# Optimization experiments

Hardware: AMD Instinct MI355X
Metric: run time of the kernel (lower is better)

Reference implementation:

```python
import jax, jax.numpy as jnp
import numpy as np

N_NODES = 50000
N_EDGES = 800000
N_PAIRS = 200000
IN_DIM = 128
HID = 64
OUT_DIM = 1


def _gat_layer(x, W, a_l, a_r, src, dst, n_nodes):
    # Single-head GAT (DGL-style): z = xW; attention logits from learned
    # left/right vectors; softmax over incoming edges of each dst node.
    z = x @ W                                   # [N, H]
    el = z @ a_l                                # [N]
    er = z @ a_r                                # [N]
    e = jax.nn.leaky_relu(el[src] + er[dst], 0.2)   # [E]
    emax = jax.ops.segment_max(e, dst, num_segments=n_nodes)  # [N]
    ex = jnp.exp(e - emax[dst])                 # [E], stable softmax numerator
    denom = jax.ops.segment_sum(ex, dst, num_segments=n_nodes)  # [N]
    msg = ex[:, None] * z[src]                  # [E, H]
    agg = jax.ops.segment_sum(msg, dst, num_segments=n_nodes)   # [N, H]
    return agg / jnp.maximum(denom, 1e-9)[:, None]


def setup_inputs() -> dict:
    key = jax.random.key(0)
    ks = jax.random.split(key, 10)
    feat = jax.random.normal(ks[0], (N_NODES, IN_DIM), dtype=jnp.float32)
    src = jax.random.randint(ks[1], (N_EDGES,), 0, N_NODES, dtype=jnp.int32)
    dst = jax.random.randint(ks[2], (N_EDGES,), 0, N_NODES, dtype=jnp.int32)
    # query pairs: take existing edges so the has_edges_between mask is true
    pair_src = src[:N_PAIRS]
    pair_dst = dst[:N_PAIRS]
    s1 = 1.0 / np.sqrt(IN_DIM)
    s2 = 1.0 / np.sqrt(HID)
    W1 = jax.random.normal(ks[3], (IN_DIM, HID), dtype=jnp.float32) * s1
    al1 = jax.random.normal(ks[4], (HID,), dtype=jnp.float32) * s2
    ar1 = jax.random.normal(ks[5], (HID,), dtype=jnp.float32) * s2
    W2 = jax.random.normal(ks[6], (HID, HID), dtype=jnp.float32) * s2
    al2 = jax.random.normal(ks[7], (HID,), dtype=jnp.float32) * s2
    ar2 = jax.random.normal(ks[8], (HID,), dtype=jnp.float32) * s2
    Wc = jax.random.normal(ks[9], (2 * HID, OUT_DIM), dtype=jnp.float32) * s2
    bc = jnp.zeros((OUT_DIM,), dtype=jnp.float32)
    return {"feat": feat, "W1": W1, "al1": al1, "ar1": ar1,
            "W2": W2, "al2": al2, "ar2": ar2, "Wc": Wc, "bc": bc,
            "src": src, "dst": dst, "pair_src": pair_src, "pair_dst": pair_dst}


def reference(feat, W1, al1, ar1, W2, al2, ar2, Wc, bc, src, dst, pair_src, pair_dst):
    src = src.astype(jnp.int32)
    dst = dst.astype(jnp.int32)
    # two hetero GAT layers (single ntype -> mean aggregate is identity) + ReLU
    h = jax.nn.relu(_gat_layer(feat, W1, al1, ar1, src, dst, N_NODES))
    h = jax.nn.relu(_gat_layer(h, W2, al2, ar2, src, dst, N_NODES))
    # has_edges_between(pair_src, pair_dst): membership test via sorted edge keys
    ekeys = src.astype(jnp.int64) * N_NODES + dst.astype(jnp.int64)
    skeys = jnp.sort(ekeys)
    pkeys = pair_src.astype(jnp.int64) * N_NODES + pair_dst.astype(jnp.int64)
    idx = jnp.clip(jnp.searchsorted(skeys, pkeys), 0, N_EDGES - 1)
    mask = (skeys[idx] == pkeys)                 # [P] bool
    # gather endpoint embeddings, concat, classify, sigmoid; invalid rows -> 0
    hs = h[pair_src]                             # [P, H]
    hd = h[pair_dst]                             # [P, H]
    h_pair = jnp.concatenate([hs, hd], axis=1)   # [P, 2H]
    out = jax.nn.sigmoid(h_pair @ Wc + bc)       # [P, OUT]
    return out * mask[:, None].astype(out.dtype)
```

## Files before the change

### kernel.cpp

```cpp
#include <hip/hip_runtime.h>
#include <cstdint>

#define N_NODES 50000
#define N_EDGES 800000
#define N_PAIRS 200000
#define IN_DIM 128
#define HID 64
#define N_WAVES_GEMM (N_NODES / 16)
#define NB1 196
#define CHUNK ((N_EDGES + NB1 - 1) / NB1)
#define MHIST (NB1 * NB1)
#define SBG ((MHIST + 255) / 256)

typedef __attribute__((ext_vector_type(8))) short bf16x8;
typedef __attribute__((ext_vector_type(4))) float f32x4;

__device__ __forceinline__ unsigned short bf16_rne(float f) {
    unsigned u = __float_as_uint(f);
    unsigned t = u + 0x7FFFu + ((u >> 16) & 1u);
    return (unsigned short)(t >> 16);
}
__device__ __forceinline__ void bf2f(unsigned u, float& a, float& b) {
    a = __uint_as_float(u << 16);
    b = __uint_as_float(u & 0xFFFF0000u);
}

__global__ __launch_bounds__(256) void hist_prep(
    const int* __restrict__ dst, int* __restrict__ histHi,
    const float* __restrict__ W1, const float* __restrict__ W2,
    unsigned short* __restrict__ w1hi, unsigned short* __restrict__ w1lo,
    unsigned short* __restrict__ w2hi, unsigned short* __restrict__ w2lo)
{
    const int t = threadIdx.x, b = blockIdx.x;
    if (b < NB1) {
        __shared__ int hist[256];
        hist[t] = 0; __syncthreads();
        const int beg = b * CHUNK, end = min(beg + CHUNK, N_EDGES);
        for (int e = beg + t; e < end; e += 256) atomicAdd(&hist[dst[e] >> 8], 1);
        __syncthreads();
        if (t < NB1) histHi[t * NB1 + b] = hist[t];
    } else {
        int tid = (b - NB1) * 256 + t;
        if (tid < 8192) {
            int jj = tid & 7, lane = (tid >> 3) & 63, tt = (tid >> 9) & 3, ks = tid >> 11;
            int k = ks * 32 + (lane >> 4) * 8 + jj;
            int n = tt * 16 + (lane & 15);
            float f = W1[k * HID + n];
            unsigned short hi = bf16_rne(f);
            float fhi = __uint_as_float(((unsigned)hi) << 16);
            w1hi[tid] = hi;
            w1lo[tid] = bf16_rne(f - fhi);
        }
        if (tid < 4096) {
            int jj = tid & 7, lane = (tid >> 3) & 63, tt = (tid >> 9) & 3, ks = tid >> 11;
            int k = ks * 32 + (lane >> 4) * 8 + jj;
            int n = tt * 16 + (lane & 15);
            float f = W2[k * HID + n];
            unsigned short hi = bf16_rne(f);
            float fhi = __uint_as_float(((unsigned)hi) << 16);
            w2hi[tid] = hi;
            w2lo[tid] = bf16_rne(f - fhi);
        }
    }
}

__global__ __launch_bounds__(256) void gemm_mfma_f(
    const float* __restrict__ x,
    const unsigned short* __restrict__ whi, const unsigned short* __restrict__ wlo,
    const float* __restrict__ al, const float* __restrict__ ar,
    unsigned short* __restrict__ z, float* __restrict__ el, float* __restrict__ er)
{
    const int lane = threadIdx.x;
    const int wave = blockIdx.x * 4 + threadIdx.y;
    if (wave >= N_WAVES_GEMM) return;
    const int i0 = wave * 16;
    const int m = lane & 15, quad = lane >> 4;

    f32x4 acc[4] = {{0.f,0.f,0.f,0.f},{0.f,0.f,0.f,0.f},{0.f,0.f,0.f,0.f},{0.f,0.f,0.f,0.f}};
    const float* xrow = x + (size_t)(i0 + m) * IN_DIM;

    #pragma unroll 1
    for (int ks = 0; ks < 4; ++ks) {
        const float4 xv0 = *(const float4*)&xrow[ks * 32 + quad * 8];
        const float4 xv1 = *(const float4*)&xrow[ks * 32 + quad * 8 + 4];
        float xs[8] = {xv0.x, xv0.y, xv0.z, xv0.w, xv1.x, xv1.y, xv1.z, xv1.w};
        bf16x8 ahi, alo;
        #pragma unroll
        for (int jj = 0; jj < 8; ++jj) {
            unsigned short hb = bf16_rne(xs[jj]);
            float fhi = __uint_as_float(((unsigned)hb) << 16);
            ahi[jj] = (short)hb;
            alo[jj] = (short)bf16_rne(xs[jj] - fhi);
        }
        #pragma unroll
        for (int t = 0; t < 4; ++t) {
            const bf16x8 bhi = *(const bf16x8*)&whi[(((ks * 4 + t) * 64) + lane) * 8];
            const bf16x8 blo = *(const bf16x8*)&wlo[(((ks * 4 + t) * 64) + lane) * 8];
            acc[t] = __builtin_amdgcn_mfma_f32_16x16x32_bf16(ahi, bhi, acc[t], 0, 0, 0);
            acc[t] = __builtin_amdgcn_mfma_f32_16x16x32_bf16(ahi, blo, acc[t], 0, 0, 0);
            acc[t] = __builtin_amdgcn_mfma_f32_16x16x32_bf16(alo, bhi, acc[t], 0, 0, 0);
        }
    }

    #pragma unroll
    for (int r = 0; r < 4; ++r) {
        const int row = quad * 4 + r;
        float se = 0.f, sr = 0.f;
        #pragma unroll
        for (int t = 0; t < 4; ++t) {
            float v = acc[t][r];
            z[(size_t)(i0 + row) * HID + t * 16 + m] = bf16_rne(v);
            se = fmaf(v, al[t * 16 + m], se);
            sr = fmaf(v, ar[t * 16 + m], sr);
        }
        #pragma unroll
        for (int off = 1; off < 16; off <<= 1) {
            se += __shfl_xor(se, off, 64);
            sr += __shfl_xor(sr, off, 64);
        }
        if (m == 0) { el[i0 + row] = se; er[i0 + row] = sr; }
    }
}

__global__ __launch_bounds__(256) void gemm_mfma_b(
    const unsigned short* __restrict__ x,
    const unsigned short* __restrict__ whi, const unsigned short* __restrict__ wlo,
    const float* __restrict__ al, const float* __restrict__ ar,
    unsigned short* __restrict__ z, float* __restrict__ el, float* __restrict__ er)
{
    const int lane = threadIdx.x;
    const int wave = blockIdx.x * 4 + threadIdx.y;
    if (wave >= N_WAVES_GEMM) return;
    const int i0 = wave * 16;
    const int m = lane & 15, quad = lane >> 4;

    f32x4 acc[4] = {{0.f,0.f,0.f,0.f},{0.f,0.f,0.f,0.f},{0.f,0.f,0.f,0.f},{0.f,0.f,0.f,0.f}};
    const unsigned short* xrow = x + (size_t)(i0 + m) * HID;

    #pragma unroll 1
    for (int ks = 0; ks < 2; ++ks) {
        const bf16x8 a = *(const bf16x8*)&xrow[ks * 32 + quad * 8];
        #pragma unroll
        for (int t = 0; t < 4; ++t) {
            const bf16x8 bhi = *(const bf16x8*)&whi[(((ks * 4 + t) * 64) + lane) * 8];
            const bf16x8 blo = *(const bf16x8*)&wlo[(((ks * 4 + t) * 64) + lane) * 8];
            acc[t] = __builtin_amdgcn_mfma_f32_16x16x32_bf16(a, bhi, acc[t], 0, 0, 0);
            acc[t] = __builtin_amdgcn_mfma_f32_16x16x32_bf16(a, blo, acc[t], 0, 0, 0);
        }
    }

    #pragma unroll
    for (int r = 0; r < 4; ++r) {
        const int row = quad * 4 + r;
        float se = 0.f, sr = 0.f;
        #pragma unroll
        for (int t = 0; t < 4; ++t) {
            float v = acc[t][r];
            z[(size_t)(i0 + row) * HID + t * 16 + m] = bf16_rne(v);
            se = fmaf(v, al[t * 16 + m], se);
            sr = fmaf(v, ar[t * 16 + m], sr);
        }
        #pragma unroll
        for (int off = 1; off < 16; off <<= 1) {
            se += __shfl_xor(se, off, 64);
            sr += __shfl_xor(sr, off, 64);
        }
        if (m == 0) { el[i0 + row] = se; er[i0 + row] = sr; }
    }
}

__global__ __launch_bounds__(256) void scan1g(
    const int* __restrict__ in, int* __restrict__ ex, int* __restrict__ bsums, int n)
{
    __shared__ int sh[256];
    const int t = threadIdx.x;
    const int i = blockIdx.x * 256 + t;
    int v = (i < n) ? in[i] : 0;
    sh[t] = v; __syncthreads();
    #pragma unroll
    for (int off = 1; off < 256; off <<= 1) {
        int x = sh[t];
        int a = (t >= off) ? sh[t - off] : 0;
        __syncthreads();
        sh[t] = x + a;
        __syncthreads();
    }
    if (i < n) ex[i] = sh[t] - v;
    if (t == 255) bsums[blockIdx.x] = sh[255];
}

__global__ __launch_bounds__(256) void scan2g(int* __restrict__ bsums, int nb)
{
    __shared__ int sh[256];
    const int t = threadIdx.x;
    int v = (t < nb) ? bsums[t] : 0;
    sh[t] = v; __syncthreads();
    #pragma unroll
    for (int off = 1; off < 256; off <<= 1) {
        int x = sh[t];
        int a = (t >= off) ? sh[t - off] : 0;
        __syncthreads();
        sh[t] = x + a;
        __syncthreads();
    }
    if (t < nb) bsums[t] = sh[t] - v;
}

__global__ __launch_bounds__(256) void scatter_hi(
    const int* __restrict__ src, const int* __restrict__ dst,
    const int* __restrict__ histEx, const int* __restrict__ bsums,
    unsigned* __restrict__ pairs)
{
    __shared__ int base[256];
    const int t = threadIdx.x, b = blockIdx.x;
    if (t < NB1) {
        int idx = t * NB1 + b;
        base[t] = histEx[idx] + bsums[idx >> 8];
    }
    __syncthreads();
    const int beg = b * CHUNK, end = min(beg + CHUNK, N_EDGES);
    for (int e = beg + t; e < end; e += 256) {
        int s = src[e], d = dst[e];
        int pos = atomicAdd(&base[d >> 8], 1);
        pairs[pos] = ((unsigned)s << 16) | (unsigned)d;
    }
}

__global__ __launch_bounds__(256) void seg_sort(
    const unsigned* __restrict__ pairs, const int* __restrict__ histEx,
    const int* __restrict__ bsums,
    int* __restrict__ row_start, int* __restrict__ csr_src)
{
    __shared__ int hist[256], sc[256], offs[256];
    const int t = threadIdx.x, b = blockIdx.x;
    const int i0 = b * NB1;
    const int segStart = histEx[i0] + bsums[i0 >> 8];
    int segEnd = N_EDGES;
    if (b < NB1 - 1) {
        const int i1 = (b + 1) * NB1;
        segEnd = histEx[i1] + bsums[i1 >> 8];
    }
    hist[t] = 0; __syncthreads();
    for (int i = segStart + t; i < segEnd; i += 256)
        atomicAdd(&hist[pairs[i] & 255], 1);
    __syncthreads();
    int v = hist[t]; sc[t] = v; __syncthreads();
    #pragma unroll
    for (int off = 1; off < 256; off <<= 1) {
        int x = sc[t];
        int a = (t >= off) ? sc[t - off] : 0;
        __syncthreads();
        sc[t] = x + a;
        __syncthreads();
    }
    const int excl = sc[t] - v;
    offs[t] = segStart + excl;
    const int node = b * 256 + t;
    if (node <= N_NODES) row_start[node] = segStart + excl;
    __syncthreads();
    for (int i = segStart + t; i < segEnd; i += 256) {
        unsigned p = pairs[i];
        int pos = atomicAdd(&offs[p & 255], 1);
        csr_src[pos] = (int)(p >> 16);
    }
}

__global__ __launch_bounds__(256) void node_agg(
    const int* __restrict__ row_start, const int* __restrict__ csr_src,
    const float* __restrict__ el, const float* __restrict__ er,
    const unsigned short* __restrict__ z, unsigned short* __restrict__ h)
{
    const int lane = threadIdx.x;
    const int i = blockIdx.x * 4 + threadIdx.y;
    if (i >= N_NODES) return;
    const int rb = row_start[i], re = row_start[i + 1];
    const float er_i = er[i];
    const int es = lane >> 3;
    const int fl = lane & 7;

    float acc[8] = {0.f,0.f,0.f,0.f,0.f,0.f,0.f,0.f};
    float den = 0.f;

    int eA = rb + es;        bool vA = eA < re;
    int eB = eA + 8;         bool vB = eB < re;
    int sA = vA ? csr_src[eA] : 0;
    int sB = vB ? csr_src[eB] : 0;
    float elA = el[sA];
    uint4 zA = ((const uint4*)(z + (size_t)sA * HID))[fl];

    for (int e0 = rb; e0 < re; e0 += 8) {
        const int eC = e0 + 16 + es;
        const bool vC = eC < re;
        const int sC = vC ? csr_src[eC] : 0;
        const float elB = el[sB];
        const uint4 zB = ((const uint4*)(z + (size_t)sB * HID))[fl];

        float x = elA + er_i;
        float lr = x > 0.f ? x : 0.2f * x;
        float ex = vA ? __expf(lr) : 0.f;
        float z0, z1, z2, z3, z4, z5, z6, z7;
        bf2f(zA.x, z0, z1); bf2f(zA.y, z2, z3);
        bf2f(zA.z, z4, z5); bf2f(zA.w, z6, z7);
        acc[0] = fmaf(ex, z0, acc[0]); acc[1] = fmaf(ex, z1, acc[1]);
        acc[2] = fmaf(ex, z2, acc[2]); acc[3] = fmaf(ex, z3, acc[3]);
        acc[4] = fmaf(ex, z4, acc[4]); acc[5] = fmaf(ex, z5, acc[5]);
        acc[6] = fmaf(ex, z6, acc[6]); acc[7] = fmaf(ex, z7, acc[7]);
        den += ex;

        sA = sB; vA = vB; elA = elB; zA = zB;
        sB = sC; vB = vC;
    }
    #pragma unroll
    for (int off = 8; off < 64; off <<= 1) {
        #pragma unroll
        for (int q = 0; q < 8; ++q) acc[q] += __shfl_xor(acc[q], off, 64);
        den += __shfl_xor(den, off, 64);
    }
    if (es == 0) {
        float inv = 1.f / fmaxf(den, 1e-9f);
        unsigned short o[8];
        #pragma unroll
        for (int q = 0; q < 8; ++q) o[q] = bf16_rne(fmaxf(acc[q] * inv, 0.f));
        uint4 pk;
        pk.x = (unsigned)o[0] | ((unsigned)o[1] << 16);
        pk.y = (unsigned)o[2] | ((unsigned)o[3] << 16);
        pk.z = (unsigned)o[4] | ((unsigned)o[5] << 16);
        pk.w = (unsigned)o[6] | ((unsigned)o[7] << 16);
        ((uint4*)(h + (size_t)i * HID))[fl] = pk;
    }
}

__global__ __launch_bounds__(256) void pair_head(
    const int* __restrict__ ps, const int* __restrict__ pd,
    const unsigned short* __restrict__ h, const float* __restrict__ Wc,
    const float* __restrict__ bc, const int* __restrict__ row_start,
    const int* __restrict__ csr_src, float* __restrict__ out)
{
    const int lane = threadIdx.x;
    const int p = blockIdx.x * 8 + threadIdx.y * 2 + (lane >> 5);
    if (p >= N_PAIRS) return;
    const int r = lane & 31;
    const int which = r >> 4;
    const int f4 = r & 15;
    int s = ps[p], d = pd[p];
    int node = which ? d : s;
    const uint2 hv = ((const uint2*)(h + (size_t)node * HID))[f4];
    float h0, h1, h2, h3;
    bf2f(hv.x, h0, h1); bf2f(hv.y, h2, h3);
    const float4 wv = *(const float4*)&Wc[which * HID + f4 * 4];
    float v = h0 * wv.x + h1 * wv.y + h2 * wv.z + h3 * wv.w;

    const int rb = row_start[d], re = row_start[d + 1];
    int found = 0;
    for (int e = rb + r; e < re; e += 32) found |= (csr_src[e] == s) ? 1 : 0;

    #pragma unroll
    for (int off = 1; off < 32; off <<= 1) {
        v += __shfl_xor(v, off, 64);
        found |= __shfl_xor(found, off, 64);
    }
    if (r == 0) {
        float sg = 1.f / (1.f + __expf(-(v + bc[0])));
        out[p] = found ? sg : 0.f;
    }
}

extern "C" void kernel_launch(void* const* d_in, const int* in_sizes, int n_in,
                              void* d_out, int out_size, void* d_ws, size_t ws_size,
                              hipStream_t stream)
{
    const float* feat = (const float*)d_in[0];
    const float* W1   = (const float*)d_in[1];
    const float* al1  = (const float*)d_in[2];
    const float* ar1  = (const float*)d_in[3];
    const float* W2   = (const float*)d_in[4];
    const float* al2  = (const float*)d_in[5];
    const float* ar2  = (const float*)d_in[6];
    const float* Wc   = (const float*)d_in[7];
    const float* bc   = (const float*)d_in[8];
    const int* src    = (const int*)d_in[9];
    const int* dst    = (const int*)d_in[10];
    const int* psrc   = (const int*)d_in[11];
    const int* pdst   = (const int*)d_in[12];
    float* out = (float*)d_out;

    char* ws = (char*)d_ws;
    unsigned short* z  = (unsigned short*)ws;  ws += (size_t)N_NODES * HID * 2;
    unsigned short* h1 = (unsigned short*)ws;  ws += (size_t)N_NODES * HID * 2;
    float* el = (float*)ws;               ws += (size_t)N_NODES * 4;
    float* er = (float*)ws;               ws += (size_t)N_NODES * 4;
    int* row_start = (int*)ws;            ws += (size_t)(N_NODES + 1) * 4;
    int* histHi = (int*)ws;               ws += (size_t)MHIST * 4;
    int* bsumsA = (int*)ws;               ws += (size_t)(SBG + 1) * 4;
    ws = (char*)(((uintptr_t)ws + 255) & ~(uintptr_t)255);
    unsigned* pairs = (unsigned*)ws;      ws += (size_t)N_EDGES * 4;
    int* csr_src = (int*)ws;              ws += (size_t)N_EDGES * 4;
    unsigned short* w1hi = (unsigned short*)ws;  ws += 8192 * 2;
    unsigned short* w1lo = (unsigned short*)ws;  ws += 8192 * 2;
    unsigned short* w2hi = (unsigned short*)ws;  ws += 4096 * 2;
    unsigned short* w2lo = (unsigned short*)ws;  ws += 4096 * 2;

    dim3 b64x4(64, 4);
    const int MB = (N_WAVES_GEMM + 3) / 4;

    hist_prep<<<NB1 + 32, 256, 0, stream>>>(dst, histHi, W1, W2, w1hi, w1lo, w2hi, w2lo);
    scan1g<<<SBG, 256, 0, stream>>>(histHi, histHi, bsumsA, MHIST);
    scan2g<<<1, 256, 0, stream>>>(bsumsA, SBG);
    scatter_hi<<<NB1, 256, 0, stream>>>(src, dst, histHi, bsumsA, pairs);
    seg_sort<<<NB1, 256, 0, stream>>>(pairs, histHi, bsumsA, row_start, csr_src);

    gemm_mfma_f<<<MB, b64x4, 0, stream>>>(feat, w1hi, w1lo, al1, ar1, z, el, er);
    node_agg<<<(N_NODES + 3) / 4, b64x4, 0, stream>>>(row_start, csr_src, el, er, z, h1);

    gemm_mfma_b<<<MB, b64x4, 0, stream>>>(h1, w2hi, w2lo, al2, ar2, z, el, er);
    node_agg<<<(N_NODES + 3) / 4, b64x4, 0, stream>>>(row_start, csr_src, el, er, z, h1);

    pair_head<<<N_PAIRS / 8, b64x4, 0, stream>>>(psrc, pdst, h1, Wc, bc, row_start, csr_src, out);
}
```

Before: 212.9 us.

## Merge scan with first GEMM, fold classifier into aggregation, restructure pair head

```diff
diff --git a/kernel.cpp b/kernel.cpp
--- a/kernel.cpp
+++ b/kernel.cpp
@@ -11,6 +11,9 @@
 #define CHUNK ((N_EDGES + NB1 - 1) / NB1)
 #define MHIST (NB1 * NB1)
 #define SBG ((MHIST + 255) / 256)
+#define MB_GEMM ((N_WAVES_GEMM + 3) / 4)
+#define NODE_BLOCKS ((N_NODES + 3) / 4)
+#define MEMBER_BLOCKS (N_PAIRS / 32)
 
 typedef __attribute__((ext_vector_type(8))) short bf16x8;
 typedef __attribute__((ext_vector_type(4))) float f32x4;
@@ -64,18 +67,15 @@
     }
 }
 
-__global__ __launch_bounds__(256) void gemm_mfma_f(
+__device__ __forceinline__ void gemm1_body(
+    int wave, int lane,
     const float* __restrict__ x,
     const unsigned short* __restrict__ whi, const unsigned short* __restrict__ wlo,
     const float* __restrict__ al, const float* __restrict__ ar,
     unsigned short* __restrict__ z, float* __restrict__ el, float* __restrict__ er)
 {
-    const int lane = threadIdx.x;
-    const int wave = blockIdx.x * 4 + threadIdx.y;
-    if (wave >= N_WAVES_GEMM) return;
     const int i0 = wave * 16;
     const int m = lane & 15, quad = lane >> 4;
-
     f32x4 acc[4] = {{0.f,0.f,0.f,0.f},{0.f,0.f,0.f,0.f},{0.f,0.f,0.f,0.f},{0.f,0.f,0.f,0.f}};
     const float* xrow = x + (size_t)(i0 + m) * IN_DIM;
 
@@ -101,7 +101,6 @@
             acc[t] = __builtin_amdgcn_mfma_f32_16x16x32_bf16(alo, bhi, acc[t], 0, 0, 0);
         }
     }
-
     #pragma unroll
     for (int r = 0; r < 4; ++r) {
         const int row = quad * 4 + r;
@@ -122,60 +121,41 @@
     }
 }
 
-__global__ __launch_bounds__(256) void gemm_mfma_b(
-    const unsigned short* __restrict__ x,
+__global__ __launch_bounds__(256) void scan_gemm1(
+    int* __restrict__ histHi, int* __restrict__ bsums,
+    const float* __restrict__ x,
     const unsigned short* __restrict__ whi, const unsigned short* __restrict__ wlo,
     const float* __restrict__ al, const float* __restrict__ ar,
     unsigned short* __restrict__ z, float* __restrict__ el, float* __restrict__ er)
 {
-    const int lane = threadIdx.x;
-    const int wave = blockIdx.x * 4 + threadIdx.y;
-    if (wave >= N_WAVES_GEMM) return;
-    const int i0 = wave * 16;
-    const int m = lane & 15, quad = lane >> 4;
-
-    f32x4 acc[4] = {{0.f,0.f,0.f,0.f},{0.f,0.f,0.f,0.f},{0.f,0.f,0.f,0.f},{0.f,0.f,0.f,0.f}};
-    const unsigned short* xrow = x + (size_t)(i0 + m) * HID;
-
-    #pragma unroll 1
-    for (int ks = 0; ks < 2; ++ks) {
-        const bf16x8 a = *(const bf16x8*)&xrow[ks * 32 + quad * 8];
-        #pragma unroll
-        for (int t = 0; t < 4; ++t) {
-            const bf16x8 bhi = *(const bf16x8*)&whi[(((ks * 4 + t) * 64) + lane) * 8];
-            const bf16x8 blo = *(const bf16x8*)&wlo[(((ks * 4 + t) * 64) + lane) * 8];
-            acc[t] = __builtin_amdgcn_mfma_f32_16x16x32_bf16(a, bhi, acc[t], 0, 0, 0);
-            acc[t] = __builtin_amdgcn_mfma_f32_16x16x32_bf16(a, blo, acc[t], 0, 0, 0);
-        }
-    }
-
-    #pragma unroll
-    for (int r = 0; r < 4; ++r) {
-        const int row = quad * 4 + r;
-        float se = 0.f, sr = 0.f;
-        #pragma unroll
-        for (int t = 0; t < 4; ++t) {
-            float v = acc[t][r];
-            z[(size_t)(i0 + row) * HID + t * 16 + m] = bf16_rne(v);
-            se = fmaf(v, al[t * 16 + m], se);
-            sr = fmaf(v, ar[t * 16 + m], sr);
-        }
-        #pragma unroll
-        for (int off = 1; off < 16; off <<= 1) {
-            se += __shfl_xor(se, off, 64);
-            sr += __shfl_xor(sr, off, 64);
-        }
-        if (m == 0) { el[i0 + row] = se; er[i0 + row] = sr; }
-    }
-}
-
-__global__ __launch_bounds__(256) void scan1g(
-    const int* __restrict__ in, int* __restrict__ ex, int* __restrict__ bsums, int n)
-{
-    __shared__ int sh[256];
-    const int t = threadIdx.x;
-    const int i = blockIdx.x * 256 + t;
-    int v = (i < n) ? in[i] : 0;
+    const int b = blockIdx.x;
+    if (b < SBG) {
+        __shared__ int sh[256];
+        const int t = threadIdx.y * 64 + threadIdx.x;
+        const int i = b * 256 + t;
+        int v = (i < MHIST) ? histHi[i] : 0;
+        sh[t] = v; __syncthreads();
+        #pragma unroll
+        for (int off = 1; off < 256; off <<= 1) {
+            int x2 = sh[t];
+            int a = (t >= off) ? sh[t - off] : 0;
+            __syncthreads();
+            sh[t] = x2 + a;
+            __syncthreads();
+        }
+        if (i < MHIST) histHi[i] = sh[t] - v;
+        if (t == 255) bsums[b] = sh[255];
+    } else {
+        const int wave = (b - SBG) * 4 + threadIdx.y;
+        if (wave < N_WAVES_GEMM)
+            gemm1_body(wave, threadIdx.x, x, whi, wlo, al, ar, z, el, er);
+    }
+}
+
+__device__ __forceinline__ void scan_bsums(const int* __restrict__ bsums,
+                                           int* sh, int* exb, int t)
+{
+    int v = (t < SBG) ? bsums[t] : 0;
     sh[t] = v; __syncthreads();
     #pragma unroll
     for (int off = 1; off < 256; off <<= 1) {
@@ -185,25 +165,8 @@
         sh[t] = x + a;
         __syncthreads();
     }
-    if (i < n) ex[i] = sh[t] - v;
-    if (t == 255) bsums[blockIdx.x] = sh[255];
-}
-
-__global__ __launch_bounds__(256) void scan2g(int* __restrict__ bsums, int nb)
-{
-    __shared__ int sh[256];
-    const int t = threadIdx.x;
-    int v = (t < nb) ? bsums[t] : 0;
-    sh[t] = v; __syncthreads();
-    #pragma unroll
-    for (int off = 1; off < 256; off <<= 1) {
-        int x = sh[t];
-        int a = (t >= off) ? sh[t - off] : 0;
-        __syncthreads();
-        sh[t] = x + a;
-        __syncthreads();
-    }
-    if (t < nb) bsums[t] = sh[t] - v;
+    exb[t] = sh[t] - v;
+    __syncthreads();
 }
 
 __global__ __launch_bounds__(256) void scatter_hi(
@@ -211,11 +174,12 @@
     const int* __restrict__ histEx, const int* __restrict__ bsums,
     unsigned* __restrict__ pairs)
 {
-    __shared__ int base[256];
+    __shared__ int sh[256], exb[256], base[256];
     const int t = threadIdx.x, b = blockIdx.x;
+    scan_bsums(bsums, sh, exb, t);
     if (t < NB1) {
         int idx = t * NB1 + b;
-        base[t] = histEx[idx] + bsums[idx >> 8];
+        base[t] = histEx[idx] + exb[idx >> 8];
     }
     __syncthreads();
     const int beg = b * CHUNK, end = min(beg + CHUNK, N_EDGES);
@@ -231,14 +195,15 @@
     const int* __restrict__ bsums,
     int* __restrict__ row_start, int* __restrict__ csr_src)
 {
-    __shared__ int hist[256], sc[256], offs[256];
+    __shared__ int sh[256], exb[256], hist[256], sc[256], offs[256];
     const int t = threadIdx.x, b = blockIdx.x;
+    scan_bsums(bsums, sh, exb, t);
     const int i0 = b * NB1;
-    const int segStart = histEx[i0] + bsums[i0 >> 8];
+    const int segStart = histEx[i0] + exb[i0 >> 8];
     int segEnd = N_EDGES;
     if (b < NB1 - 1) {
         const int i1 = (b + 1) * NB1;
-        segEnd = histEx[i1] + bsums[i1 >> 8];
+        segEnd = histEx[i1] + exb[i1 >> 8];
     }
     hist[t] = 0; __syncthreads();
     for (int i = segStart + t; i < segEnd; i += 256)
@@ -265,14 +230,14 @@
     }
 }
 
-__global__ __launch_bounds__(256) void node_agg(
+template <bool LAST>
+__device__ __forceinline__ void agg_body(
+    int i, int lane,
     const int* __restrict__ row_start, const int* __restrict__ csr_src,
     const float* __restrict__ el, const float* __restrict__ er,
-    const unsigned short* __restrict__ z, unsigned short* __restrict__ h)
-{
-    const int lane = threadIdx.x;
-    const int i = blockIdx.x * 4 + threadIdx.y;
-    if (i >= N_NODES) return;
+    const unsigned short* __restrict__ z, unsigned short* __restrict__ h,
+    const float* __restrict__ Wc, float* __restrict__ as, float* __restrict__ ad)
+{
     const int rb = row_start[i], re = row_start[i + 1];
     const float er_i = er[i];
     const int es = lane >> 3;
@@ -318,51 +283,131 @@
     }
     if (es == 0) {
         float inv = 1.f / fmaxf(den, 1e-9f);
-        unsigned short o[8];
-        #pragma unroll
-        for (int q = 0; q < 8; ++q) o[q] = bf16_rne(fmaxf(acc[q] * inv, 0.f));
-        uint4 pk;
-        pk.x = (unsigned)o[0] | ((unsigned)o[1] << 16);
-        pk.y = (unsigned)o[2] | ((unsigned)o[3] << 16);
-        pk.z = (unsigned)o[4] | ((unsigned)o[5] << 16);
-        pk.w = (unsigned)o[6] | ((unsigned)o[7] << 16);
-        ((uint4*)(h + (size_t)i * HID))[fl] = pk;
-    }
-}
-
-__global__ __launch_bounds__(256) void pair_head(
+        float hv[8];
+        #pragma unroll
+        for (int q = 0; q < 8; ++q) hv[q] = fmaxf(acc[q] * inv, 0.f);
+        if (LAST) {
+            float ps = 0.f, pd = 0.f;
+            #pragma unroll
+            for (int q = 0; q < 8; ++q) {
+                ps = fmaf(hv[q], Wc[fl * 8 + q], ps);
+                pd = fmaf(hv[q], Wc[HID + fl * 8 + q], pd);
+            }
+            #pragma unroll
+            for (int off = 1; off < 8; off <<= 1) {
+                ps += __shfl_xor(ps, off, 64);
+                pd += __shfl_xor(pd, off, 64);
+            }
+            if (fl == 0) { as[i] = ps; ad[i] = pd; }
+        } else {
+            unsigned short o[8];
+            #pragma unroll
+            for (int q = 0; q < 8; ++q) o[q] = bf16_rne(hv[q]);
+            uint4 pk;
+            pk.x = (unsigned)o[0] | ((unsigned)o[1] << 16);
+            pk.y = (unsigned)o[2] | ((unsigned)o[3] << 16);
+            pk.z = (unsigned)o[4] | ((unsigned)o[5] << 16);
+            pk.w = (unsigned)o[6] | ((unsigned)o[7] << 16);
+            ((uint4*)(h + (size_t)i * HID))[fl] = pk;
+        }
+    }
+}
+
+__global__ __launch_bounds__(256) void agg1_member(
+    const int* __restrict__ row_start, const int* __restrict__ csr_src,
+    const float* __restrict__ el, const float* __restrict__ er,
+    const unsigned short* __restrict__ z, unsigned short* __restrict__ h,
     const int* __restrict__ ps, const int* __restrict__ pd,
-    const unsigned short* __restrict__ h, const float* __restrict__ Wc,
-    const float* __restrict__ bc, const int* __restrict__ row_start,
-    const int* __restrict__ csr_src, float* __restrict__ out)
+    int* __restrict__ found)
+{
+    const int lane = threadIdx.x, b = blockIdx.x;
+    if (b < NODE_BLOCKS) {
+        const int i = b * 4 + threadIdx.y;
+        if (i < N_NODES)
+            agg_body<false>(i, lane, row_start, csr_src, el, er, z, h,
+                            nullptr, nullptr, nullptr);
+    } else {
+        const int r = lane & 7, g = lane >> 3;
+        const int p = (b - NODE_BLOCKS) * 32 + threadIdx.y * 8 + g;
+        const int s = ps[p], d = pd[p];
+        const int rb = row_start[d], re = row_start[d + 1];
+        int f = 0;
+        for (int e = rb + r; e < re; e += 8) f |= (csr_src[e] == s) ? 1 : 0;
+        #pragma unroll
+        for (int off = 1; off < 8; off <<= 1) f |= __shfl_xor(f, off, 64);
+        if (r == 0) found[p] = f;
+    }
+}
+
+__global__ __launch_bounds__(256) void gemm_mfma_b(
+    const unsigned short* __restrict__ x,
+    const unsigned short* __restrict__ whi, const unsigned short* __restrict__ wlo,
+    const float* __restrict__ al, const float* __restrict__ ar,
+    unsigned short* __restrict__ z, float* __restrict__ el, float* __restrict__ er)
 {
     const int lane = threadIdx.x;
-    const int p = blockIdx.x * 8 + threadIdx.y * 2 + (lane >> 5);
+    const int wave = blockIdx.x * 4 + threadIdx.y;
+    if (wave >= N_WAVES_GEMM) return;
+    const int i0 = wave * 16;
+    const int m = lane & 15, quad = lane >> 4;
+
+    f32x4 acc[4] = {{0.f,0.f,0.f,0.f},{0.f,0.f,0.f,0.f},{0.f,0.f,0.f,0.f},{0.f,0.f,0.f,0.f}};
+    const unsigned short* xrow = x + (size_t)(i0 + m) * HID;
+
+    #pragma unroll 1
+    for (int ks = 0; ks < 2; ++ks) {
+        const bf16x8 a = *(const bf16x8*)&xrow[ks * 32 + quad * 8];
+        #pragma unroll
+        for (int t = 0; t < 4; ++t) {
+            const bf16x8 bhi = *(const bf16x8*)&whi[(((ks * 4 + t) * 64) + lane) * 8];
+            const bf16x8 blo = *(const bf16x8*)&wlo[(((ks * 4 + t) * 64) + lane) * 8];
+            acc[t] = __builtin_amdgcn_mfma_f32_16x16x32_bf16(a, bhi, acc[t], 0, 0, 0);
+            acc[t] = __builtin_amdgcn_mfma_f32_16x16x32_bf16(a, blo, acc[t], 0, 0, 0);
+        }
+    }
+    #pragma unroll
+    for (int r = 0; r < 4; ++r) {
+        const int row = quad * 4 + r;
+        float se = 0.f, sr = 0.f;
+        #pragma unroll
+        for (int t = 0; t < 4; ++t) {
+            float v = acc[t][r];
+            z[(size_t)(i0 + row) * HID + t * 16 + m] = bf16_rne(v);
+            se = fmaf(v, al[t * 16 + m], se);
+            sr = fmaf(v, ar[t * 16 + m], sr);
+        }
+        #pragma unroll
+        for (int off = 1; off < 16; off <<= 1) {
+            se += __shfl_xor(se, off, 64);
+            sr += __shfl_xor(sr, off, 64);
+        }
+        if (m == 0) { el[i0 + row] = se; er[i0 + row] = sr; }
+    }
+}
+
+__global__ __launch_bounds__(256) void agg2(
+    const int* __restrict__ row_start, const int* __restrict__ csr_src,
+    const float* __restrict__ el, const float* __restrict__ er,
+    const unsigned short* __restrict__ z, const float* __restrict__ Wc,
+    float* __restrict__ as, float* __restrict__ ad)
+{
+    const int i = blockIdx.x * 4 + threadIdx.y;
+    if (i < N_NODES)
+        agg_body<true>(i, threadIdx.x, row_start, csr_src, el, er, z,
+                       nullptr, Wc, as, ad);
+}
+
+__global__ __launch_bounds__(256) void pair_tiny(
+    const int* __restrict__ ps, const int* __restrict__ pd,
+    const float* __restrict__ as, const float* __restrict__ ad,
+    const float* __restrict__ bc, const int* __restrict__ found,
+    float* __restrict__ out)
+{
+    const int p = blockIdx.x * 256 + threadIdx.x;
     if (p >= N_PAIRS) return;
-    const int r = lane & 31;
-    const int which = r >> 4;
-    const int f4 = r & 15;
-    int s = ps[p], d = pd[p];
-    int node = which ? d : s;
-    const uint2 hv = ((const uint2*)(h + (size_t)node * HID))[f4];
-    float h0, h1, h2, h3;
-    bf2f(hv.x, h0, h1); bf2f(hv.y, h2, h3);
-    const float4 wv = *(const float4*)&Wc[which * HID + f4 * 4];
-    float v = h0 * wv.x + h1 * wv.y + h2 * wv.z + h3 * wv.w;
-
-    const int rb = row_start[d], re = row_start[d + 1];
-    int found = 0;
-    for (int e = rb + r; e < re; e += 32) found |= (csr_src[e] == s) ? 1 : 0;
-
-    #pragma unroll
-    for (int off = 1; off < 32; off <<= 1) {
-        v += __shfl_xor(v, off, 64);
-        found |= __shfl_xor(found, off, 64);
-    }
-    if (r == 0) {
-        float sg = 1.f / (1.f + __expf(-(v + bc[0])));
-        out[p] = found ? sg : 0.f;
-    }
+    float v = as[ps[p]] + ad[pd[p]] + bc[0];
+    float sg = 1.f / (1.f + __expf(-v));
+    out[p] = found[p] ? sg : 0.f;
 }
 
 extern "C" void kernel_launch(void* const* d_in, const int* in_sizes, int n_in,
@@ -389,9 +434,12 @@
     unsigned short* h1 = (unsigned short*)ws;  ws += (size_t)N_NODES * HID * 2;
     float* el = (float*)ws;               ws += (size_t)N_NODES * 4;
     float* er = (float*)ws;               ws += (size_t)N_NODES * 4;
+    float* as = (float*)ws;               ws += (size_t)N_NODES * 4;
+    float* ad = (float*)ws;               ws += (size_t)N_NODES * 4;
     int* row_start = (int*)ws;            ws += (size_t)(N_NODES + 1) * 4;
     int* histHi = (int*)ws;               ws += (size_t)MHIST * 4;
     int* bsumsA = (int*)ws;               ws += (size_t)(SBG + 1) * 4;
+    int* found = (int*)ws;                ws += (size_t)N_PAIRS * 4;
     ws = (char*)(((uintptr_t)ws + 255) & ~(uintptr_t)255);
     unsigned* pairs = (unsigned*)ws;      ws += (size_t)N_EDGES * 4;
     int* csr_src = (int*)ws;              ws += (size_t)N_EDGES * 4;
@@ -401,19 +449,15 @@
     unsigned short* w2lo = (unsigned short*)ws;  ws += 4096 * 2;
 
     dim3 b64x4(64, 4);
-    const int MB = (N_WAVES_GEMM + 3) / 4;
 
     hist_prep<<<NB1 + 32, 256, 0, stream>>>(dst, histHi, W1, W2, w1hi, w1lo, w2hi, w2lo);
-    scan1g<<<SBG, 256, 0, stream>>>(histHi, histHi, bsumsA, MHIST);
-    scan2g<<<1, 256, 0, stream>>>(bsumsA, SBG);
+    scan_gemm1<<<SBG + MB_GEMM, b64x4, 0, stream>>>(histHi, bsumsA,
+        feat, w1hi, w1lo, al1, ar1, z, el, er);
     scatter_hi<<<NB1, 256, 0, stream>>>(src, dst, histHi, bsumsA, pairs);
     seg_sort<<<NB1, 256, 0, stream>>>(pairs, histHi, bsumsA, row_start, csr_src);
-
-    gemm_mfma_f<<<MB, b64x4, 0, stream>>>(feat, w1hi, w1lo, al1, ar1, z, el, er);
-    node_agg<<<(N_NODES + 3) / 4, b64x4, 0, stream>>>(row_start, csr_src, el, er, z, h1);
-
-    gemm_mfma_b<<<MB, b64x4, 0, stream>>>(h1, w2hi, w2lo, al2, ar2, z, el, er);
-    node_agg<<<(N_NODES + 3) / 4, b64x4, 0, stream>>>(row_start, csr_src, el, er, z, h1);
-
-    pair_head<<<N_PAIRS / 8, b64x4, 0, stream>>>(psrc, pdst, h1, Wc, bc, row_start, csr_src, out);
-}
+    agg1_member<<<NODE_BLOCKS + MEMBER_BLOCKS, b64x4, 0, stream>>>(
+        row_start, csr_src, el, er, z, h1, psrc, pdst, found);
+    gemm_mfma_b<<<MB_GEMM, b64x4, 0, stream>>>(h1, w2hi, w2lo, al2, ar2, z, el, er);
+    agg2<<<NODE_BLOCKS, b64x4, 0, stream>>>(row_start, csr_src, el, er, z, Wc, as, ad);
+    pair_tiny<<<(N_PAIRS + 255) / 256, 256, 0, stream>>>(psrc, pdst, as, ad, bc, found, out);
+}
```

Result: faster. 194.0 us (-8.9%).
